# Performance work log

Measured on AMD Instinct MI355X. Metric: run time of the kernel, lower is better.

## Reference

```python
import jax, jax.numpy as jnp
import numpy as np

EPS = 1e-5

def rmsnorm(x, w):
    var = jnp.mean(x * x, axis=-1, keepdims=True)
    return x * jax.lax.rsqrt(var + EPS) * w


def setup_inputs() -> dict:
    key = jax.random.key(0)
    B, L, dim = 4, 2048, 1024
    d_inner, d_state, d_conv, dt_rank = 2 * dim, 16, 4, dim // 16
    ks = jax.random.split(key, 8)
    g = lambda k, shape, scale: (jax.random.normal(k, shape, jnp.float32) * scale)
    return {
        "x": g(ks[0], (B, L, dim), 1.0),
        "rms_w": jnp.ones((dim,), jnp.float32),
        "in_proj": g(ks[1], (dim, 2 * d_inner), dim ** -0.5),
        "conv_w": g(ks[2], (d_inner, d_conv), 0.25),
        "conv_b": jnp.zeros((d_inner,), jnp.float32),
        "x_proj": g(ks[3], (d_inner, dt_rank + 2 * d_state), d_inner ** -0.5),
        "dt_w": g(ks[4], (dt_rank, d_inner), dt_rank ** -0.5),
        # inverse-softplus(0.01): softplus(dt_b) ~ 0.01 at init, standard Mamba dt init
        "dt_b": jnp.full((d_inner,), float(np.log(np.expm1(0.01))), jnp.float32),
        # S4D-real init: A_n = -(n+1)
        "A_log": jnp.log(jnp.broadcast_to(jnp.arange(1, d_state + 1, dtype=jnp.float32), (d_inner, d_state))).copy(),
        "D": jnp.ones((d_inner,), jnp.float32),
        "out_proj": g(ks[5], (d_inner, dim), d_inner ** -0.5),
    }


def _mamba_block(x, rms_w, in_proj, conv_w, conv_b, x_proj, dt_w, dt_b, A_log, D, out_proj):
    B, L, dim = x.shape
    d_inner, K = conv_w.shape
    d_state = A_log.shape[1]
    dt_rank = dt_w.shape[0]

    xn = rmsnorm(x, rms_w)
    xz = xn @ in_proj                      # [B,L,2*d_inner]
    xi, z = jnp.split(xz, 2, axis=-1)

    # causal depthwise conv1d over L
    xc = jax.lax.conv_general_dilated(
        xi.transpose(0, 2, 1),             # [B,C,L]
        conv_w[:, None, :],                # [C,1,K]
        window_strides=(1,), padding=[(K - 1, 0)],
        feature_group_count=d_inner,
    ).transpose(0, 2, 1) + conv_b
    xi = jax.nn.silu(xc)                   # [B,L,d_inner]

    dbc = xi @ x_proj                      # [B,L,dt_rank+2*d_state]
    dt, Bm, Cm = jnp.split(dbc, [dt_rank, dt_rank + d_state], axis=-1)
    delta = jax.nn.softplus(dt @ dt_w + dt_b)  # [B,L,d_inner]
    A = -jnp.exp(A_log)                    # [d_inner,d_state]

    def step(h, inputs):
        d_t, x_t, B_t, C_t = inputs        # [B,d_inner],[B,d_inner],[B,d_state],[B,d_state]
        dA = jnp.exp(d_t[..., None] * A)   # [B,d_inner,d_state]
        h = dA * h + (d_t * x_t)[..., None] * B_t[:, None, :]
        y = jnp.einsum('bds,bs->bd', h, C_t)
        return h, y

    h0 = jnp.zeros((B, d_inner, d_state), x.dtype)
    xs = (delta.transpose(1, 0, 2), xi.transpose(1, 0, 2),
          Bm.transpose(1, 0, 2), Cm.transpose(1, 0, 2))
    _, ys = jax.lax.scan(step, h0, xs)     # ys: [L,B,d_inner]

    y = ys.transpose(1, 0, 2) + xi * D     # D skip connection
    y = y * jax.nn.silu(z)                 # output gate
    return x + y @ out_proj                # residual


def reference(x, rms_w, in_proj, conv_w, conv_b, x_proj, dt_w, dt_b, A_log, D, out_proj):
    return _mamba_block(x, rms_w, in_proj, conv_w, conv_b, x_proj, dt_w, dt_b, A_log, D, out_proj)
```

## Files before the change

### kernel.cpp

```cpp
#include <hip/hip_runtime.h>
#include <hip/hip_bf16.h>
#include <math.h>


#define ROWS 8192
#define DIM 1024
#define DINNER 2048
#define DSTATE 16
#define DTRANK 64
#define LSEQ 2048
#define NCHUNK 32
#define LCHUNK 64

#define LOG2E 1.4426950408889634f

typedef unsigned short ushort;
typedef __attribute__((ext_vector_type(8))) short short8;
typedef __attribute__((ext_vector_type(4))) float float4v;

__device__ inline ushort f2bf(float f) {
    __hip_bfloat16 h = __float2bfloat16(f);
    return *reinterpret_cast<ushort*>(&h);
}
__device__ inline float bf2f(ushort u) {
    union { unsigned int i; float f; } w; w.i = ((unsigned int)u) << 16; return w.f;
}

__device__ inline float fexp2(float x) {
#if __has_builtin(__builtin_amdgcn_exp2f)
    return __builtin_amdgcn_exp2f(x);
#else
    return __expf(x * 0.69314718056f);
#endif
}

__device__ inline void dma16(const void* g, void* l) {
    __builtin_amdgcn_global_load_lds(
        (const __attribute__((address_space(1))) unsigned int*)g,
        (__attribute__((address_space(3))) unsigned int*)l, 16, 0, 0);
}

template <int N> __device__ inline void vwait() {
    if constexpr (N == 0)      asm volatile("s_waitcnt vmcnt(0)" ::: "memory");
    else if constexpr (N == 3) asm volatile("s_waitcnt vmcnt(3)" ::: "memory");
    else if constexpr (N == 4) asm volatile("s_waitcnt vmcnt(4)" ::: "memory");
    else if constexpr (N == 6) asm volatile("s_waitcnt vmcnt(6)" ::: "memory");
    else if constexpr (N == 8) asm volatile("s_waitcnt vmcnt(8)" ::: "memory");
    else static_assert(N < 0, "unsupported vmcnt literal");
}

__global__ __launch_bounds__(256)
void prep_kernel(const float* __restrict__ in_proj, ushort* __restrict__ bt1,
                 const float* __restrict__ out_proj, ushort* __restrict__ bt2,
                 const float* __restrict__ x_proj, ushort* __restrict__ bt3,
                 const float* __restrict__ dt_w, ushort* __restrict__ bt4,
                 const float* __restrict__ x, const float* __restrict__ rms_w,
                 ushort* __restrict__ xn, float* __restrict__ dbc) {
    __shared__ float tld[32][33];
    __shared__ float red[4];
    int bid = blockIdx.x, tid = threadIdx.x;
    if (bid < 6464) {
        const float* in; ushort* outT; int R, C, bx, by;
        if (bid < 4096)      { in = in_proj;  outT = bt1; R = 1024; C = 4096; bx = bid & 127; by = bid >> 7; }
        else if (bid < 6144) { int t = bid - 4096; in = out_proj; outT = bt2; R = 2048; C = 1024; bx = t & 31; by = t >> 5; }
        else if (bid < 6336) { int t = bid - 6144; in = x_proj;  outT = bt3; R = 2048; C = 96;  bx = t % 3;  by = t / 3; }
        else                 { int t = bid - 6336; in = dt_w;    outT = bt4; R = 64;   C = 2048; bx = t & 63; by = t >> 6; }
        int tx = tid & 31, ty = tid >> 5;
#pragma unroll
        for (int k = 0; k < 4; ++k)
            tld[ty + k * 8][tx] = in[(long)(by * 32 + ty + k * 8) * C + bx * 32 + tx];
        __syncthreads();
#pragma unroll
        for (int k = 0; k < 4; ++k)
            outT[(long)(bx * 32 + ty + k * 8) * R + by * 32 + tx] = f2bf(tld[tx][ty + k * 8]);
    } else if (bid < 14656) {
        int row = bid - 6464;
        float4 xv = ((const float4*)(x + (long)row * DIM))[tid];
        float ss = xv.x * xv.x + xv.y * xv.y + xv.z * xv.z + xv.w * xv.w;
        for (int off = 32; off > 0; off >>= 1) ss += __shfl_down(ss, off);
        if ((tid & 63) == 0) red[tid >> 6] = ss;
        __syncthreads();
        float scale = rsqrtf((red[0] + red[1] + red[2] + red[3]) / DIM + 1e-5f);
        float4 wv = ((const float4*)rms_w)[tid];
        ushort4 ov;
        ov.x = f2bf(xv.x * scale * wv.x);
        ov.y = f2bf(xv.y * scale * wv.y);
        ov.z = f2bf(xv.z * scale * wv.z);
        ov.w = f2bf(xv.w * scale * wv.w);
        ((ushort4*)xn)[(long)row * 256 + tid] = ov;
    } else {
        int idx = (bid - 14656) * 256 + tid;
        float4 z = {0.f, 0.f, 0.f, 0.f};
        ((float4*)dbc)[idx] = z;
    }
}

template <int MW, int NW, int MF, int NF, int SUBP, int EPI>
__global__ __launch_bounds__(MW * NW * 64, 2)
void gemm_ring(const ushort* __restrict__ A, int lda,
               const ushort* __restrict__ Bt, int ldbt,
               void* __restrict__ Cv, int ldc, int K,
               const float* __restrict__ aux) {
    constexpr int W    = MW * NW;
    constexpr int BLKM = MW * MF * 16;
    constexpr int BLKN = NW * NF * 16;
    constexpr int TILE = (BLKM + BLKN) * 32;
    constexpr int NA   = BLKM / (16 * W);
    constexpr int NB   = BLKN / (16 * W);
    constexpr int DPT  = NA + NB;
    constexpr int MH   = MF / SUBP;
    __shared__ __align__(16) ushort lds[4 * TILE];

    const int tid  = threadIdx.x;
    const int w    = tid >> 6, lane = tid & 63;
    const int wm   = w / NW,   wn   = w % NW;
    const int quad = lane >> 4, l16 = lane & 15;
    const long row0 = (long)blockIdx.y * BLKM;
    const long col0 = (long)blockIdx.x * BLKN;

    const ushort* gA[NA];
    const ushort* gB[NB];
#pragma unroll
    for (int i = 0; i < NA; ++i)
        gA[i] = A + (row0 + (w + i * W) * 16 + l16) * lda + quad * 8;
#pragma unroll
    for (int i = 0; i < NB; ++i)
        gB[i] = Bt + (col0 + (w + i * W) * 16 + l16) * ldbt + quad * 8;

    const int NT = K >> 5;
    float4v acc[MF][NF] = {};

    auto stageA = [&](int kt) {
        ushort* lb = lds + (kt & 3) * TILE;
        const int ko = kt << 5;
#pragma unroll
        for (int i = 0; i < NA; ++i)
            dma16(gA[i] + ko, lb + (w + i * W) * 512);
    };
    auto stageB = [&](int kt) {
        ushort* lb = lds + (kt & 3) * TILE + BLKM * 32;
        const int ko = kt << 5;
#pragma unroll
        for (int i = 0; i < NB; ++i)
            dma16(gB[i] + ko, lb + (w + i * W) * 512);
    };
    auto tailwait = [&](int t) {
        if (t + 3 < NT)      vwait<2 * DPT>();
        else if (t + 2 < NT) vwait<DPT>();
        else                 vwait<0>();
    };

    stageA(0); stageB(0); stageA(1); stageB(1); stageA(2); stageB(2);
    vwait<2 * DPT>();
    __builtin_amdgcn_s_barrier();

    for (int t = 0; t < NT; ++t) {
        const ushort* lb  = lds + (t & 3) * TILE;
        const ushort* lbB = lb + BLKM * 32;
        const bool stg = (t + 3 < NT);
        short8 af[MF], bfr[NF];

#pragma unroll
        for (int n = 0; n < NF; ++n)
            bfr[n] = *reinterpret_cast<const short8*>(
                &lbB[(wn * NF + n) * 512 + lane * 8]);
#pragma unroll
        for (int m = 0; m < MH; ++m)
            af[m] = *reinterpret_cast<const short8*>(
                &lb[(wm * MF + m) * 512 + lane * 8]);
        if (stg) { stageA(t + 3); if (SUBP == 1) stageB(t + 3); }
        __builtin_amdgcn_s_barrier();
        asm volatile("s_waitcnt lgkmcnt(0)" ::: "memory");
        __builtin_amdgcn_sched_barrier(0);
        __builtin_amdgcn_s_setprio(1);
#pragma unroll
        for (int m = 0; m < MH; ++m)
#pragma unroll
            for (int n = 0; n < NF; ++n)
                acc[m][n] = __builtin_amdgcn_mfma_f32_16x16x32_bf16(
                    af[m], bfr[n], acc[m][n], 0, 0, 0);
        __builtin_amdgcn_s_setprio(0);

        if (SUBP == 1) {
            tailwait(t);
            if (t < NT - 1) __builtin_amdgcn_s_barrier();
        } else {
            __builtin_amdgcn_s_barrier();
#pragma unroll
            for (int m = MH; m < MF; ++m)
                af[m] = *reinterpret_cast<const short8*>(
                    &lb[(wm * MF + m) * 512 + lane * 8]);
            if (stg) stageB(t + 3);
            __builtin_amdgcn_s_barrier();
            asm volatile("s_waitcnt lgkmcnt(0)" ::: "memory");
            __builtin_amdgcn_sched_barrier(0);
            __builtin_amdgcn_s_setprio(1);
#pragma unroll
            for (int m = MH; m < MF; ++m)
#pragma unroll
                for (int n = 0; n < NF; ++n)
                    acc[m][n] = __builtin_amdgcn_mfma_f32_16x16x32_bf16(
                        af[m], bfr[n], acc[m][n], 0, 0, 0);
            __builtin_amdgcn_s_setprio(0);
            tailwait(t);
            if (t < NT - 1) __builtin_amdgcn_s_barrier();
        }
    }

#pragma unroll
    for (int m = 0; m < MF; ++m) {
#pragma unroll
        for (int n = 0; n < NF; ++n) {
            long rbase = row0 + wm * (MF * 16) + m * 16 + quad * 4;
            long c = col0 + wn * (NF * 16) + n * 16 + l16;
#pragma unroll
            for (int r = 0; r < 4; ++r) {
                float v = acc[m][n][r];
                long idx = (rbase + r) * (long)ldc + c;
                if (EPI == 2) ((float*)Cv)[idx] = v + aux[idx];
                else          ((ushort*)Cv)[idx] = f2bf(v);
            }
        }
    }
}

__global__ __launch_bounds__(256)
void xproj_conv_gemm(const ushort* __restrict__ xz,
                     const float* __restrict__ cw, const float* __restrict__ cb,
                     const ushort* __restrict__ bt3,
                     float* __restrict__ dbc) {
    __shared__ __align__(16) ushort As[128][32];
    __shared__ __align__(16) ushort Bs[128][32];
    int tid = threadIdx.x;
    int wave = tid >> 6, lane = tid & 63;
    int wm = wave >> 1, wn = wave & 1;
    int quad = lane >> 4, l16 = lane & 15;
    int row0 = blockIdx.y * 128;
    int ks0 = blockIdx.x * 512;
    int srow = tid >> 2, sseg = tid & 3;

    int r0 = (wave * 2 + 0) * 16 + (lane >> 2);
    int r1 = (wave * 2 + 1) * 16 + (lane >> 2);
    int ksl = (lane & 3) * 8;
    const ushort* b0 = bt3 + (long)r0 * 2048 + ks0 + ksl;
    const ushort* b1 = bt3 + (long)r1 * 2048 + ks0 + ksl;
    ushort* lB0 = &Bs[(wave * 2 + 0) * 16][0];
    ushort* lB1 = &Bs[(wave * 2 + 1) * 16][0];

    float4v acc[4][4] = {};

    for (int k0 = 0; k0 < 512; k0 += 32) {
        dma16(b0 + k0, lB0);
        dma16(b1 + k0, lB1);
#pragma unroll
        for (int it = 0; it < 2; ++it) {
            int r = srow + it * 64;
            long row = row0 + r;
            int l = (int)(row & (LSEQ - 1));
            int cch = ks0 + k0 + sseg * 8;
            short8 v[4];
#pragma unroll
            for (int t = 0; t < 4; ++t) {
                if (l - 3 + t >= 0) v[t] = *(const short8*)&xz[(row - 3 + t) * 4096 + cch];
                else { short8 zz = {0,0,0,0,0,0,0,0}; v[t] = zz; }
            }
            ushort o[8];
#pragma unroll
            for (int j = 0; j < 8; ++j) {
                float4 w = ((const float4*)cw)[cch + j];
                float a = cb[cch + j]
                        + bf2f((ushort)v[0][j]) * w.x + bf2f((ushort)v[1][j]) * w.y
                        + bf2f((ushort)v[2][j]) * w.z + bf2f((ushort)v[3][j]) * w.w;
                a = a / (1.f + __expf(-a));
                o[j] = f2bf(a);
            }
            *(short8*)&As[r][sseg * 8] = *(const short8*)o;
        }
        __syncthreads();

        short8 afrag[4], bfrag[4];
#pragma unroll
        for (int i = 0; i < 4; ++i)
            afrag[i] = *reinterpret_cast<const short8*>(&As[wm * 64 + i * 16 + l16][quad * 8]);
#pragma unroll
        for (int j = 0; j < 4; ++j)
            bfrag[j] = *reinterpret_cast<const short8*>(&Bs[wn * 64 + j * 16 + l16][quad * 8]);
#pragma unroll
        for (int i = 0; i < 4; ++i)
#pragma unroll
            for (int j = 0; j < 4; ++j)
                acc[i][j] = __builtin_amdgcn_mfma_f32_16x16x32_bf16(
                    afrag[i], bfrag[j], acc[i][j], 0, 0, 0);
        __syncthreads();
    }
#pragma unroll
    for (int i = 0; i < 4; ++i) {
#pragma unroll
        for (int j = 0; j < 4; ++j) {
            int rbase = row0 + wm * 64 + i * 16 + quad * 4;
            int c = wn * 64 + j * 16 + l16;
            if (c < 96) {
#pragma unroll
                for (int r = 0; r < 4; ++r)
                    atomicAdd(&dbc[(long)(rbase + r) * 96 + c], acc[i][j][r]);
            }
        }
    }
}

__global__ __launch_bounds__(256)
void mfma_gemm_dt(const float* __restrict__ A, int lda,
                  const ushort* __restrict__ Bt, int ldbt,
                  ushort* __restrict__ C, int ldc, int K,
                  const float* __restrict__ aux) {
    __shared__ __align__(16) ushort As[128][40];
    __shared__ __align__(16) ushort Bs[128][40];
    int tid = threadIdx.x;
    int wave = tid >> 6, lane = tid & 63;
    int wm = wave >> 1, wn = wave & 1;
    int quad = lane >> 4, l16 = lane & 15;
    int row0 = blockIdx.y * 128, col0 = blockIdx.x * 128;
    int srow = tid >> 2, sseg = tid & 3;

    float4v acc[4][4] = {};

    for (int k0 = 0; k0 < K; k0 += 32) {
#pragma unroll
        for (int it = 0; it < 2; ++it) {
            int r = srow + it * 64;
            const float* ap = A + (long)(row0 + r) * lda + k0 + sseg * 8;
            ushort tmp[8];
#pragma unroll
            for (int j = 0; j < 8; ++j) tmp[j] = f2bf(ap[j]);
            *reinterpret_cast<short8*>(&As[r][sseg * 8]) =
                *reinterpret_cast<const short8*>(tmp);
            const ushort* bp = Bt + (long)(col0 + r) * ldbt + k0 + sseg * 8;
            *reinterpret_cast<short8*>(&Bs[r][sseg * 8]) =
                *reinterpret_cast<const short8*>(bp);
        }
        __syncthreads();
        short8 afrag[4], bfrag[4];
#pragma unroll
        for (int i = 0; i < 4; ++i)
            afrag[i] = *reinterpret_cast<const short8*>(&As[wm * 64 + i * 16 + l16][quad * 8]);
#pragma unroll
        for (int j = 0; j < 4; ++j)
            bfrag[j] = *reinterpret_cast<const short8*>(&Bs[wn * 64 + j * 16 + l16][quad * 8]);
#pragma unroll
        for (int i = 0; i < 4; ++i)
#pragma unroll
            for (int j = 0; j < 4; ++j)
                acc[i][j] = __builtin_amdgcn_mfma_f32_16x16x32_bf16(
                    afrag[i], bfrag[j], acc[i][j], 0, 0, 0);
        __syncthreads();
    }
#pragma unroll
    for (int i = 0; i < 4; ++i) {
#pragma unroll
        for (int j = 0; j < 4; ++j) {
            int rbase = row0 + wm * 64 + i * 16 + quad * 4;
            int c = col0 + wn * 64 + j * 16 + l16;
#pragma unroll
            for (int r = 0; r < 4; ++r) {
                float v = acc[i][j][r] + aux[c];
                v = (v > 20.f) ? v : __logf(1.f + __expf(v));
                C[(long)(rbase + r) * ldc + c] = f2bf(v);
            }
        }
    }
}

__global__ __launch_bounds__(256)
void scan_part1(const ushort* __restrict__ xz,
                const ushort* __restrict__ dlt,
                const float* __restrict__ dbc,
                const float* __restrict__ A_log,
                const float* __restrict__ cw, const float* __restrict__ cb,
                float* __restrict__ hbuf,
                float* __restrict__ sdbuf) {
    int c = blockIdx.y * 256 + threadIdx.x;
    int b = blockIdx.z, g = blockIdx.x;
    float A2[16];
#pragma unroll
    for (int s = 0; s < 16; ++s) A2[s] = -__expf(A_log[c * 16 + s]) * LOG2E;
    float4 w = ((const float4*)cw)[c];
    float cbc = cb[c];
    float h[16] = {};
    float sumd = 0.f;
    long row0 = (long)b * LSEQ + (long)g * LCHUNK;
    int l0 = g * LCHUNK;
    float x0 = (l0 >= 3) ? bf2f(xz[(row0 - 3) * 4096 + c]) : 0.f;
    float x1 = (l0 >= 2) ? bf2f(xz[(row0 - 2) * 4096 + c]) : 0.f;
    float x2 = (l0 >= 1) ? bf2f(xz[(row0 - 1) * 4096 + c]) : 0.f;
    long row = row0;
    for (int l = 0; l < LCHUNK; ++l, ++row) {
        float x3 = bf2f(xz[row * 4096 + c]);
        float xc = cbc + x0 * w.x + x1 * w.y + x2 * w.z + x3 * w.w;
        xc = xc / (1.f + __expf(-xc));
        x0 = x1; x1 = x2; x2 = x3;
        float d = bf2f(dlt[row * 2048 + c]);
        const float* __restrict__ bc = dbc + row * 96;
        sumd += d;
        float dx = d * xc;
#pragma unroll
        for (int s = 0; s < 16; ++s)
            h[s] = fexp2(d * A2[s]) * h[s] + dx * bc[64 + s];
    }
    long hb = ((long)(b * NCHUNK + g) * 16) * 2048 + c;
#pragma unroll
    for (int s = 0; s < 16; ++s) hbuf[hb + (long)s * 2048] = h[s];
    sdbuf[(long)(b * NCHUNK + g) * 2048 + c] = sumd;
}

__global__ __launch_bounds__(256)
void scan_part2(float* __restrict__ hbuf, const float* __restrict__ sdbuf,
                const float* __restrict__ A_log) {
    int gl = blockIdx.x * 256 + threadIdx.x;
    int c = gl & 2047, s = (gl >> 11) & 15, b = gl >> 15;
    float A2 = -__expf(A_log[c * 16 + s]) * LOG2E;
    float hrun = 0.f;
    for (int g = 0; g < NCHUNK; ++g) {
        long hi = ((long)(b * NCHUNK + g) * 16 + s) * 2048 + c;
        float hout = hbuf[hi];
        float sd = sdbuf[(long)(b * NCHUNK + g) * 2048 + c];
        hbuf[hi] = hrun;
        hrun = fexp2(A2 * sd) * hrun + hout;
    }
}

__global__ __launch_bounds__(256)
void scan_part3(const ushort* __restrict__ xz,
                ushort* __restrict__ dlt,
                const float* __restrict__ dbc,
                const float* __restrict__ A_log,
                const float* __restrict__ cw, const float* __restrict__ cb,
                const float* __restrict__ Dp,
                const float* __restrict__ hbuf) {
    int c = blockIdx.y * 256 + threadIdx.x;
    int b = blockIdx.z, g = blockIdx.x;
    float A2[16], h[16];
#pragma unroll
    for (int s = 0; s < 16; ++s) A2[s] = -__expf(A_log[c * 16 + s]) * LOG2E;
    long hb = ((long)(b * NCHUNK + g) * 16) * 2048 + c;
#pragma unroll
    for (int s = 0; s < 16; ++s) h[s] = hbuf[hb + (long)s * 2048];
    float4 w = ((const float4*)cw)[c];
    float cbc = cb[c];
    float Dc = Dp[c];
    long row0 = (long)b * LSEQ + (long)g * LCHUNK;
    int l0 = g * LCHUNK;
    float x0 = (l0 >= 3) ? bf2f(xz[(row0 - 3) * 4096 + c]) : 0.f;
    float x1 = (l0 >= 2) ? bf2f(xz[(row0 - 2) * 4096 + c]) : 0.f;
    float x2 = (l0 >= 1) ? bf2f(xz[(row0 - 1) * 4096 + c]) : 0.f;
    long row = row0;
    for (int l = 0; l < LCHUNK; ++l, ++row) {
        float x3 = bf2f(xz[row * 4096 + c]);
        float xc = cbc + x0 * w.x + x1 * w.y + x2 * w.z + x3 * w.w;
        xc = xc / (1.f + __expf(-xc));
        x0 = x1; x1 = x2; x2 = x3;
        float d = bf2f(dlt[row * 2048 + c]);
        float z = bf2f(xz[row * 4096 + 2048 + c]);
        const float* __restrict__ bc = dbc + row * 96;
        float dx = d * xc;
        float y = 0.f;
#pragma unroll
        for (int s = 0; s < 16; ++s) {
            h[s] = fexp2(d * A2[s]) * h[s] + dx * bc[64 + s];
            y += h[s] * bc[80 + s];
        }
        float yv = (y + xc * Dc) * (z / (1.f + __expf(-z)));
        dlt[row * 2048 + c] = f2bf(yv);
    }
}

extern "C" void kernel_launch(void* const* d_in, const int* in_sizes, int n_in,
                              void* d_out, int out_size, void* d_ws, size_t ws_size,
                              hipStream_t stream) {
    const float* x        = (const float*)d_in[0];
    const float* rms_w    = (const float*)d_in[1];
    const float* in_proj  = (const float*)d_in[2];
    const float* conv_w   = (const float*)d_in[3];
    const float* conv_b   = (const float*)d_in[4];
    const float* x_proj   = (const float*)d_in[5];
    const float* dt_w     = (const float*)d_in[6];
    const float* dt_b     = (const float*)d_in[7];
    const float* A_log    = (const float*)d_in[8];
    const float* Dp       = (const float*)d_in[9];
    const float* out_proj = (const float*)d_in[10];
    float* out = (float*)d_out;

    char* p = (char*)d_ws;
    ushort* xz  = (ushort*)p;   p += (size_t)ROWS * 4096 * 2;
    ushort* dlt = (ushort*)p;   p += (size_t)ROWS * 2048 * 2;
    float*  dbc = (float*)p;    p += (size_t)ROWS * 96 * 4;
    ushort* bt1 = (ushort*)p;   p += (size_t)4096 * 1024 * 2;
    ushort* bt2 = (ushort*)p;   p += (size_t)1024 * 2048 * 2;
    ushort* bt3 = (ushort*)p;   p += (size_t)128 * 2048 * 2;
    ushort* bt4 = (ushort*)p;   p += (size_t)2048 * 64 * 2;
    ushort* xn  = (ushort*)p;   p += (size_t)ROWS * 1024 * 2;
    float* sdbuf = (float*)p;   p += (size_t)4 * NCHUNK * 2048 * 4;
    float* hbuf  = (float*)xn;

    prep_kernel<<<15424, 256, 0, stream>>>(in_proj, bt1, out_proj, bt2,
                                           x_proj, bt3, dt_w, bt4,
                                           x, rms_w, xn, dbc);
    gemm_ring<2, 4, 8, 4, 2, 0><<<dim3(4096 / 256, ROWS / 256), 512, 0, stream>>>(
        xn, DIM, bt1, 1024, xz, 4096, DIM, nullptr);
    xproj_conv_gemm<<<dim3(4, ROWS / 128), 256, 0, stream>>>(
        xz, conv_w, conv_b, bt3, dbc);
    mfma_gemm_dt<<<dim3(2048 / 128, ROWS / 128), 256, 0, stream>>>(
        dbc, 96, bt4, 64, dlt, 2048, DTRANK, dt_b);
    scan_part1<<<dim3(NCHUNK, DINNER / 256, 4), 256, 0, stream>>>(
        xz, dlt, dbc, A_log, conv_w, conv_b, hbuf, sdbuf);
    scan_part2<<<512, 256, 0, stream>>>(hbuf, sdbuf, A_log);
    scan_part3<<<dim3(NCHUNK, DINNER / 256, 4), 256, 0, stream>>>(
        xz, dlt, dbc, A_log, conv_w, conv_b, Dp, hbuf);
    gemm_ring<4, 2, 4, 4, 1, 2><<<dim3(DIM / 128, ROWS / 256), 512, 0, stream>>>(
        dlt, DINNER, bt2, DINNER, out, DIM, DINNER, x);
}
```

Measured before the change: 479.2 us.

## Retile GEMM to 4 waves with 3-slot ring and XCD-aware block swizzle

Both GEMMs move to a 4-wave 128x256 tile, and the shared-memory ring drops from 4 stages to 3. The loop is always split into two sub-phases, so the later GEMM now also stages its B operand separately. Workgroup IDs are remapped so consecutive tiles land on the same XCD, which is meant to improve L2 reuse. The shallower prefetch depth and smaller blocks reduce LDS use and may raise occupancy, at the cost of less latency hiding per block.

Measured after the change: 495.0 us. +3.3%, slower.

```diff
diff --git a/kernel.cpp b/kernel.cpp
--- a/kernel.cpp
+++ b/kernel.cpp
@@ -42,10 +42,10 @@
 
 template <int N> __device__ inline void vwait() {
     if constexpr (N == 0)      asm volatile("s_waitcnt vmcnt(0)" ::: "memory");
-    else if constexpr (N == 3) asm volatile("s_waitcnt vmcnt(3)" ::: "memory");
     else if constexpr (N == 4) asm volatile("s_waitcnt vmcnt(4)" ::: "memory");
     else if constexpr (N == 6) asm volatile("s_waitcnt vmcnt(6)" ::: "memory");
     else if constexpr (N == 8) asm volatile("s_waitcnt vmcnt(8)" ::: "memory");
+    else if constexpr (N == 12) asm volatile("s_waitcnt vmcnt(12)" ::: "memory");
     else static_assert(N < 0, "unsupported vmcnt literal");
 }
 
@@ -95,7 +95,7 @@
     }
 }
 
-template <int MW, int NW, int MF, int NF, int SUBP, int EPI>
+template <int MW, int NW, int MF, int NF, int EPI>
 __global__ __launch_bounds__(MW * NW * 64, 2)
 void gemm_ring(const ushort* __restrict__ A, int lda,
                const ushort* __restrict__ Bt, int ldbt,
@@ -108,15 +108,21 @@
     constexpr int NA   = BLKM / (16 * W);
     constexpr int NB   = BLKN / (16 * W);
     constexpr int DPT  = NA + NB;
-    constexpr int MH   = MF / SUBP;
-    __shared__ __align__(16) ushort lds[4 * TILE];
+    constexpr int MH   = MF / 2;
+    __shared__ __align__(16) ushort lds[3 * TILE];
+
+    const int nwg = gridDim.x * gridDim.y;
+    int bid = blockIdx.y * gridDim.x + blockIdx.x;
+    bid = (bid & 7) * (nwg >> 3) + (bid >> 3);
+    const int bx = bid % gridDim.x;
+    const int by = bid / gridDim.x;
 
     const int tid  = threadIdx.x;
     const int w    = tid >> 6, lane = tid & 63;
     const int wm   = w / NW,   wn   = w % NW;
     const int quad = lane >> 4, l16 = lane & 15;
-    const long row0 = (long)blockIdx.y * BLKM;
-    const long col0 = (long)blockIdx.x * BLKN;
+    const long row0 = (long)by * BLKM;
+    const long col0 = (long)bx * BLKN;
 
     const ushort* gA[NA];
     const ushort* gB[NB];
@@ -130,34 +136,31 @@
     const int NT = K >> 5;
     float4v acc[MF][NF] = {};
 
-    auto stageA = [&](int kt) {
-        ushort* lb = lds + (kt & 3) * TILE;
+    auto stageA = [&](int kt, int slot) {
+        ushort* lb = lds + slot * TILE;
         const int ko = kt << 5;
 #pragma unroll
         for (int i = 0; i < NA; ++i)
             dma16(gA[i] + ko, lb + (w + i * W) * 512);
     };
-    auto stageB = [&](int kt) {
-        ushort* lb = lds + (kt & 3) * TILE + BLKM * 32;
+    auto stageB = [&](int kt, int slot) {
+        ushort* lb = lds + slot * TILE + BLKM * 32;
         const int ko = kt << 5;
 #pragma unroll
         for (int i = 0; i < NB; ++i)
             dma16(gB[i] + ko, lb + (w + i * W) * 512);
     };
-    auto tailwait = [&](int t) {
-        if (t + 3 < NT)      vwait<2 * DPT>();
-        else if (t + 2 < NT) vwait<DPT>();
-        else                 vwait<0>();
-    };
-
-    stageA(0); stageB(0); stageA(1); stageB(1); stageA(2); stageB(2);
-    vwait<2 * DPT>();
+
+    stageA(0, 0); stageB(0, 0); stageA(1, 1); stageB(1, 1);
+    vwait<DPT>();
     __builtin_amdgcn_s_barrier();
 
+    int s = 0;
     for (int t = 0; t < NT; ++t) {
-        const ushort* lb  = lds + (t & 3) * TILE;
+        const ushort* lb  = lds + s * TILE;
         const ushort* lbB = lb + BLKM * 32;
-        const bool stg = (t + 3 < NT);
+        const bool stg = (t + 2 < NT);
+        const int ss = (s >= 1) ? s - 1 : 2;
         short8 af[MF], bfr[NF];
 
 #pragma unroll
@@ -168,7 +171,7 @@
         for (int m = 0; m < MH; ++m)
             af[m] = *reinterpret_cast<const short8*>(
                 &lb[(wm * MF + m) * 512 + lane * 8]);
-        if (stg) { stageA(t + 3); if (SUBP == 1) stageB(t + 3); }
+        if (stg) stageA(t + 2, ss);
         __builtin_amdgcn_s_barrier();
         asm volatile("s_waitcnt lgkmcnt(0)" ::: "memory");
         __builtin_amdgcn_sched_barrier(0);
@@ -180,31 +183,27 @@
                 acc[m][n] = __builtin_amdgcn_mfma_f32_16x16x32_bf16(
                     af[m], bfr[n], acc[m][n], 0, 0, 0);
         __builtin_amdgcn_s_setprio(0);
-
-        if (SUBP == 1) {
-            tailwait(t);
-            if (t < NT - 1) __builtin_amdgcn_s_barrier();
-        } else {
-            __builtin_amdgcn_s_barrier();
-#pragma unroll
-            for (int m = MH; m < MF; ++m)
-                af[m] = *reinterpret_cast<const short8*>(
-                    &lb[(wm * MF + m) * 512 + lane * 8]);
-            if (stg) stageB(t + 3);
-            __builtin_amdgcn_s_barrier();
-            asm volatile("s_waitcnt lgkmcnt(0)" ::: "memory");
-            __builtin_amdgcn_sched_barrier(0);
-            __builtin_amdgcn_s_setprio(1);
-#pragma unroll
-            for (int m = MH; m < MF; ++m)
-#pragma unroll
-                for (int n = 0; n < NF; ++n)
-                    acc[m][n] = __builtin_amdgcn_mfma_f32_16x16x32_bf16(
-                        af[m], bfr[n], acc[m][n], 0, 0, 0);
-            __builtin_amdgcn_s_setprio(0);
-            tailwait(t);
-            if (t < NT - 1) __builtin_amdgcn_s_barrier();
-        }
+        __builtin_amdgcn_s_barrier();
+
+#pragma unroll
+        for (int m = MH; m < MF; ++m)
+            af[m] = *reinterpret_cast<const short8*>(
+                &lb[(wm * MF + m) * 512 + lane * 8]);
+        if (stg) stageB(t + 2, ss);
+        __builtin_amdgcn_s_barrier();
+        asm volatile("s_waitcnt lgkmcnt(0)" ::: "memory");
+        __builtin_amdgcn_sched_barrier(0);
+        __builtin_amdgcn_s_setprio(1);
+#pragma unroll
+        for (int m = MH; m < MF; ++m)
+#pragma unroll
+            for (int n = 0; n < NF; ++n)
+                acc[m][n] = __builtin_amdgcn_mfma_f32_16x16x32_bf16(
+                    af[m], bfr[n], acc[m][n], 0, 0, 0);
+        __builtin_amdgcn_s_setprio(0);
+        if (stg) vwait<DPT>(); else vwait<0>();
+        if (t < NT - 1) __builtin_amdgcn_s_barrier();
+        s = (s == 2) ? 0 : s + 1;
     }
 
 #pragma unroll
@@ -504,7 +503,7 @@
     prep_kernel<<<15424, 256, 0, stream>>>(in_proj, bt1, out_proj, bt2,
                                            x_proj, bt3, dt_w, bt4,
                                            x, rms_w, xn, dbc);
-    gemm_ring<2, 4, 8, 4, 2, 0><<<dim3(4096 / 256, ROWS / 256), 512, 0, stream>>>(
+    gemm_ring<1, 4, 8, 4, 0><<<dim3(4096 / 256, ROWS / 128), 256, 0, stream>>>(
         xn, DIM, bt1, 1024, xz, 4096, DIM, nullptr);
     xproj_conv_gemm<<<dim3(4, ROWS / 128), 256, 0, stream>>>(
         xz, conv_w, conv_b, bt3, dbc);
@@ -515,6 +514,6 @@
     scan_part2<<<512, 256, 0, stream>>>(hbuf, sdbuf, A_log);
     scan_part3<<<dim3(NCHUNK, DINNER / 256, 4), 256, 0, stream>>>(
         xz, dlt, dbc, A_log, conv_w, conv_b, Dp, hbuf);
-    gemm_ring<4, 2, 4, 4, 1, 2><<<dim3(DIM / 128, ROWS / 256), 512, 0, stream>>>(
+    gemm_ring<1, 4, 8, 4, 2><<<dim3(DIM / 256, ROWS / 128), 256, 0, stream>>>(
         dlt, DINNER, bt2, DINNER, out, DIM, DINNER, x);
 }
```

## Software-pipeline LDS fragment loads across k-iterations in GEMM ring kernel

Applied to the files above, without the earlier changes.

Restructures the GEMM main loop so fragments for the next k-tile (first half of A and all of B) are prefetched from LDS during the second half of the current tile's MFMAs, using ping-pong B register buffers and a loop unrolled by two. It cuts the per-iteration barrier count from two to one and issues the A and B global-to-LDS DMA together. The intent is to hide LDS read latency behind matrix-core work and reduce synchronization stalls. In exchange it raises register pressure and relies on a hand-tuned lgkmcnt/vmcnt accounting, and the unroll by two assumes the tile count is even.

Measured after the change: 479.8 us. About the same (+0.1%).

```diff
diff --git a/kernel.cpp b/kernel.cpp
--- a/kernel.cpp
+++ b/kernel.cpp
@@ -95,7 +95,7 @@
     }
 }
 
-template <int MW, int NW, int MF, int NF, int SUBP, int EPI>
+template <int MW, int NW, int MF, int NF, int EPI>
 __global__ __launch_bounds__(MW * NW * 64, 2)
 void gemm_ring(const ushort* __restrict__ A, int lda,
                const ushort* __restrict__ Bt, int ldbt,
@@ -108,7 +108,7 @@
     constexpr int NA   = BLKM / (16 * W);
     constexpr int NB   = BLKN / (16 * W);
     constexpr int DPT  = NA + NB;
-    constexpr int MH   = MF / SUBP;
+    constexpr int MH   = MF / 2;
     __shared__ __align__(16) ushort lds[4 * TILE];
 
     const int tid  = threadIdx.x;
@@ -129,6 +129,7 @@
 
     const int NT = K >> 5;
     float4v acc[MF][NF] = {};
+    short8 afN[MH], afX[MF - MH], bfrE[NF], bfrO[NF];
 
     auto stageA = [&](int kt) {
         ushort* lb = lds + (kt & 3) * TILE;
@@ -144,67 +145,69 @@
         for (int i = 0; i < NB; ++i)
             dma16(gB[i] + ko, lb + (w + i * W) * 512);
     };
-    auto tailwait = [&](int t) {
-        if (t + 3 < NT)      vwait<2 * DPT>();
-        else if (t + 2 < NT) vwait<DPT>();
-        else                 vwait<0>();
-    };
 
     stageA(0); stageB(0); stageA(1); stageB(1); stageA(2); stageB(2);
-    vwait<2 * DPT>();
+    vwait<DPT>();
     __builtin_amdgcn_s_barrier();
-
-    for (int t = 0; t < NT; ++t) {
-        const ushort* lb  = lds + (t & 3) * TILE;
-        const ushort* lbB = lb + BLKM * 32;
-        const bool stg = (t + 3 < NT);
-        short8 af[MF], bfr[NF];
-
-#pragma unroll
-        for (int n = 0; n < NF; ++n)
-            bfr[n] = *reinterpret_cast<const short8*>(
-                &lbB[(wn * NF + n) * 512 + lane * 8]);
+#pragma unroll
+    for (int m = 0; m < MH; ++m)
+        afN[m] = *reinterpret_cast<const short8*>(
+            &lds[(wm * MF + m) * 512 + lane * 8]);
+#pragma unroll
+    for (int n = 0; n < NF; ++n)
+        bfrE[n] = *reinterpret_cast<const short8*>(
+            &lds[BLKM * 32 + (wn * NF + n) * 512 + lane * 8]);
+
+    auto ITER = [&](short8 (&bcur)[NF], short8 (&bnxt)[NF], int t) {
+        const ushort* lb = lds + (t & 3) * TILE;
+#pragma unroll
+        for (int m = 0; m < MF - MH; ++m)
+            afX[m] = *reinterpret_cast<const short8*>(
+                &lb[(wm * MF + MH + m) * 512 + lane * 8]);
+        if (t + 3 < NT) { stageA(t + 3); stageB(t + 3); }
+        __builtin_amdgcn_sched_barrier(0);
+        __builtin_amdgcn_s_setprio(1);
 #pragma unroll
         for (int m = 0; m < MH; ++m)
-            af[m] = *reinterpret_cast<const short8*>(
-                &lb[(wm * MF + m) * 512 + lane * 8]);
-        if (stg) { stageA(t + 3); if (SUBP == 1) stageB(t + 3); }
-        __builtin_amdgcn_s_barrier();
+#pragma unroll
+            for (int n = 0; n < NF; ++n)
+                acc[m][n] = __builtin_amdgcn_mfma_f32_16x16x32_bf16(
+                    afN[m], bcur[n], acc[m][n], 0, 0, 0);
+        __builtin_amdgcn_s_setprio(0);
+        __builtin_amdgcn_sched_barrier(0);
+        if (t < NT - 1) {
+            const ushort* nb  = lds + ((t + 1) & 3) * TILE;
+            const ushort* nbB = nb + BLKM * 32;
+#pragma unroll
+            for (int m = 0; m < MH; ++m)
+                afN[m] = *reinterpret_cast<const short8*>(
+                    &nb[(wm * MF + m) * 512 + lane * 8]);
+#pragma unroll
+            for (int n = 0; n < NF; ++n)
+                bnxt[n] = *reinterpret_cast<const short8*>(
+                    &nbB[(wn * NF + n) * 512 + lane * 8]);
+            asm volatile("s_waitcnt lgkmcnt(%0)" :: "i"(MH + NF) : "memory");
+        } else {
+            asm volatile("s_waitcnt lgkmcnt(0)" ::: "memory");
+        }
+        __builtin_amdgcn_sched_barrier(0);
+        __builtin_amdgcn_s_setprio(1);
+#pragma unroll
+        for (int m = 0; m < MF - MH; ++m)
+#pragma unroll
+            for (int n = 0; n < NF; ++n)
+                acc[MH + m][n] = __builtin_amdgcn_mfma_f32_16x16x32_bf16(
+                    afX[m], bcur[n], acc[MH + m][n], 0, 0, 0);
+        __builtin_amdgcn_s_setprio(0);
+        if (t + 3 < NT) vwait<DPT>(); else vwait<0>();
         asm volatile("s_waitcnt lgkmcnt(0)" ::: "memory");
         __builtin_amdgcn_sched_barrier(0);
-        __builtin_amdgcn_s_setprio(1);
-#pragma unroll
-        for (int m = 0; m < MH; ++m)
-#pragma unroll
-            for (int n = 0; n < NF; ++n)
-                acc[m][n] = __builtin_amdgcn_mfma_f32_16x16x32_bf16(
-                    af[m], bfr[n], acc[m][n], 0, 0, 0);
-        __builtin_amdgcn_s_setprio(0);
-
-        if (SUBP == 1) {
-            tailwait(t);
-            if (t < NT - 1) __builtin_amdgcn_s_barrier();
-        } else {
-            __builtin_amdgcn_s_barrier();
-#pragma unroll
-            for (int m = MH; m < MF; ++m)
-                af[m] = *reinterpret_cast<const short8*>(
-                    &lb[(wm * MF + m) * 512 + lane * 8]);
-            if (stg) stageB(t + 3);
-            __builtin_amdgcn_s_barrier();
-            asm volatile("s_waitcnt lgkmcnt(0)" ::: "memory");
-            __builtin_amdgcn_sched_barrier(0);
-            __builtin_amdgcn_s_setprio(1);
-#pragma unroll
-            for (int m = MH; m < MF; ++m)
-#pragma unroll
-                for (int n = 0; n < NF; ++n)
-                    acc[m][n] = __builtin_amdgcn_mfma_f32_16x16x32_bf16(
-                        af[m], bfr[n], acc[m][n], 0, 0, 0);
-            __builtin_amdgcn_s_setprio(0);
-            tailwait(t);
-            if (t < NT - 1) __builtin_amdgcn_s_barrier();
-        }
+        if (t < NT - 1) __builtin_amdgcn_s_barrier();
+    };
+
+    for (int t = 0; t < NT; t += 2) {
+        ITER(bfrE, bfrO, t);
+        ITER(bfrO, bfrE, t + 1);
     }
 
 #pragma unroll
@@ -504,7 +507,7 @@
     prep_kernel<<<15424, 256, 0, stream>>>(in_proj, bt1, out_proj, bt2,
                                            x_proj, bt3, dt_w, bt4,
                                            x, rms_w, xn, dbc);
-    gemm_ring<2, 4, 8, 4, 2, 0><<<dim3(4096 / 256, ROWS / 256), 512, 0, stream>>>(
+    gemm_ring<2, 4, 8, 4, 0><<<dim3(4096 / 256, ROWS / 256), 512, 0, stream>>>(
         xn, DIM, bt1, 1024, xz, 4096, DIM, nullptr);
     xproj_conv_gemm<<<dim3(4, ROWS / 128), 256, 0, stream>>>(
         xz, conv_w, conv_b, bt3, dbc);
@@ -515,6 +518,6 @@
     scan_part2<<<512, 256, 0, stream>>>(hbuf, sdbuf, A_log);
     scan_part3<<<dim3(NCHUNK, DINNER / 256, 4), 256, 0, stream>>>(
         xz, dlt, dbc, A_log, conv_w, conv_b, Dp, hbuf);
-    gemm_ring<4, 2, 4, 4, 1, 2><<<dim3(DIM / 128, ROWS / 256), 512, 0, stream>>>(
+    gemm_ring<4, 2, 4, 4, 2><<<dim3(DIM / 128, ROWS / 256), 512, 0, stream>>>(
         dlt, DINNER, bt2, DINNER, out, DIM, DINNER, x);
 }
```
